# Performance work log

Measured on AMD Instinct MI355X. Metric: run time of the kernel, lower is better.

Reference implementation:

```python
import jax, jax.numpy as jnp
import numpy as np

# Model dims derived from layers=[1024,2048,2048,2048,2048]
B = 4096
SUM_EVEN = 4096  # 0 + 2048 + 2048
SUM_ODD = 4096   # 2048 + 2048
D1 = 2048        # layers[1]: width of Ux
BLK = 2048


def rho(x):
    return jax.nn.sigmoid(4.0 * (x - 0.5))


def make_mask():
    # Staircase block pattern from layer_slices():
    # (rows 0:2048, cols 0:2048), (rows 0:2048, cols 2048:4096), (rows 2048:4096, cols 2048:4096)
    m = np.zeros((SUM_EVEN, SUM_ODD), dtype=np.float32)
    m[0:BLK, 0:BLK] = 1.0
    m[0:BLK, BLK:2 * BLK] = 1.0
    m[BLK:2 * BLK, BLK:2 * BLK] = 1.0
    return jnp.asarray(m)


def setup_inputs() -> dict:
    key = jax.random.key(0)
    k1, k2, k3 = jax.random.split(key, 3)
    xavier_std = 0.02  # ~ sqrt(2/(2048+2048)) per block
    W_mask = make_mask()
    W_tensor = jax.random.normal(k1, (SUM_EVEN, SUM_ODD), jnp.float32) * xavier_std
    W_tensor = W_tensor * W_mask  # enforce staircase sparsity at init
    return {
        "Ux": jax.random.normal(k2, (B, D1), jnp.float32),
        "s": jax.random.normal(k3, (B, SUM_EVEN), jnp.float32),
        "W_tensor": W_tensor,
        "b_even": jnp.zeros((1, SUM_EVEN), jnp.float32),
        "b_odd": jnp.zeros((1, SUM_ODD), jnp.float32),
        "W_mask": W_mask,
    }


def reference(Ux, s, W_tensor, b_even, b_odd, W_mask):
    # s_new = rho(rho(s) @ W + b_odd [+ Ux on first D1 cols]) @ W.T + b_even
    W = W_tensor * W_mask  # masked staircase matrix
    s_odd = rho(s) @ W + b_odd                 # [B, SUM_ODD]
    s_odd = s_odd.at[:, :D1].add(Ux)           # x only feeds first hidden layer
    return rho(s_odd) @ W.T + b_even           # [B, SUM_EVEN]
```

## Files before the change

### kernel.cpp

```cpp
#include <hip/hip_runtime.h>
#include <hip/hip_bf16.h>


#define N_DIM 4096
#define D1_DIM 2048

typedef short short8 __attribute__((ext_vector_type(8)));
typedef float f32x4 __attribute__((ext_vector_type(4)));

__device__ __forceinline__ float rho_f(float x) {
    return 1.0f / (1.0f + __expf(2.0f - 4.0f * x));
}

__device__ __forceinline__ unsigned short f2bf(float x) {
    unsigned int u = __builtin_bit_cast(unsigned int, x);
    u += 0x7fffu + ((u >> 16) & 1u);
    return (unsigned short)(u >> 16);
}

__device__ __forceinline__ void gl_lds16(const unsigned short* g, void* l) {
    __builtin_amdgcn_global_load_lds(
        (const __attribute__((address_space(1))) void*)g,
        (__attribute__((address_space(3))) void*)l, 16, 0, 0);
}

__global__ void prep_rs_kernel(const float* __restrict__ s,
                               unsigned short* __restrict__ Rs, int n8) {
    int t = blockIdx.x * blockDim.x + threadIdx.x;
    int stride = gridDim.x * blockDim.x;
    for (int i = t; i < n8; i += stride) {
        float4 a = ((const float4*)s)[2 * i];
        float4 b = ((const float4*)s)[2 * i + 1];
        unsigned int r0 = f2bf(rho_f(a.x)) | ((unsigned int)f2bf(rho_f(a.y)) << 16);
        unsigned int r1 = f2bf(rho_f(a.z)) | ((unsigned int)f2bf(rho_f(a.w)) << 16);
        unsigned int r2 = f2bf(rho_f(b.x)) | ((unsigned int)f2bf(rho_f(b.y)) << 16);
        unsigned int r3 = f2bf(rho_f(b.z)) | ((unsigned int)f2bf(rho_f(b.w)) << 16);
        uint4 o; o.x = r0; o.y = r1; o.z = r2; o.w = r3;
        ((uint4*)Rs)[i] = o;
    }
}

__global__ void prep_w_kernel(const float* __restrict__ W,
                              unsigned short* __restrict__ Wb,
                              unsigned short* __restrict__ WTb) {
    if (blockIdx.y * 32 >= D1_DIM && blockIdx.x * 32 < D1_DIM) return;
    __shared__ unsigned short t[32][33];
    int x = blockIdx.x * 32 + threadIdx.x;
    #pragma unroll
    for (int r = 0; r < 4; r++) {
        int y = blockIdx.y * 32 + threadIdx.y + r * 8;
        size_t idx = (size_t)y * N_DIM + x;
        unsigned short b = f2bf(W[idx]);
        Wb[idx] = b;
        t[threadIdx.y + r * 8][threadIdx.x] = b;
    }
    __syncthreads();
    #pragma unroll
    for (int r = 0; r < 4; r++) {
        int yy = threadIdx.y + r * 8;
        int orow = blockIdx.x * 32 + yy;
        int ocol = blockIdx.y * 32 + threadIdx.x;
        WTb[(size_t)orow * N_DIM + ocol] = t[threadIdx.x][yy];
    }
}

template<int MODE>
__global__ __launch_bounds__(512, 2) void gemm_kernel(
    const unsigned short* __restrict__ A,
    const unsigned short* __restrict__ Bt,
    void* __restrict__ Out,
    const float* __restrict__ Ux,
    const float* __restrict__ bias) {
    __shared__ __align__(16) char lds[163840];

    const int id = blockIdx.x;
    const int wg = ((id & 7) << 5) | (id >> 3);
    const int by = wg >> 4, bx = wg & 15;
    const int brow = by << 8, bcol = bx << 8;

    const int tid = threadIdx.x;
    const int w = tid >> 6;
    const int L = tid & 63;
    const int wr = w >> 2;
    const int wc = w & 3;
    const int fr = L & 15;
    const int fq = L >> 4;
    const int swz = fr & 7;

    int kbeg, kend;
    if (MODE == 1) { kbeg = 0; kend = (bcol < D1_DIM) ? D1_DIM : N_DIM; }
    else           { kbeg = (bcol < D1_DIM) ? 0 : D1_DIM; kend = N_DIM; }

    const int srl = w * 8 + (L >> 3);
    const int schunk8 = ((L & 7) ^ (L >> 3)) << 3;
    const int wbase = w * 1024;
#define STAGE2(mat, gb, h, kcol, base) do {                                    \
        const unsigned short* g0_ = (mat) +                                    \
            (size_t)((gb) + (h) * 128 + srl) * N_DIM + (kcol) + schunk8;       \
        gl_lds16(g0_, lds + (base) + (h) * 16384 + wbase);                     \
        gl_lds16(g0_ + 64 * N_DIM, lds + (base) + (h) * 16384 + 8192 + wbase); \
    } while (0)

    short8 af[2][4], bf0[2][2], bf1[2][2];
#define LDA_Q(ab, qm) do {                                                     \
        _Pragma("unroll") for (int s_ = 0; s_ < 2; ++s_)                       \
        _Pragma("unroll") for (int m_ = 0; m_ < 4; ++m_) {                     \
            const int R_ = wr * 128 + (qm) * 64 + m_ * 16 + fr;                \
            af[s_][m_] = *(const short8*)(lds + (ab) + R_ * 128 +              \
                (((4 * s_ + fq) ^ swz) << 4)); }                               \
    } while (0)
#define LDB_Q(bb, qn, dst) do {                                                \
        _Pragma("unroll") for (int s_ = 0; s_ < 2; ++s_)                       \
        _Pragma("unroll") for (int n_ = 0; n_ < 2; ++n_) {                     \
            const int R_ = wc * 64 + (qn) * 32 + n_ * 16 + fr;                 \
            dst[s_][n_] = *(const short8*)(lds + (bb) + R_ * 128 +             \
                (((4 * s_ + fq) ^ swz) << 4)); }                               \
    } while (0)

    f32x4 acc[8][4];
    #pragma unroll
    for (int i = 0; i < 8; i++)
        #pragma unroll
        for (int j = 0; j < 4; j++)
            acc[i][j] = (f32x4){0.f, 0.f, 0.f, 0.f};

#define MFMA_Q(qm, qn, bfr) do {                                               \
        __builtin_amdgcn_s_setprio(1);                                         \
        _Pragma("unroll") for (int s_ = 0; s_ < 2; ++s_)                       \
        _Pragma("unroll") for (int m_ = 0; m_ < 4; ++m_)                       \
        _Pragma("unroll") for (int n_ = 0; n_ < 2; ++n_)                       \
            acc[(qm) * 4 + m_][(qn) * 2 + n_] =                                \
                __builtin_amdgcn_mfma_f32_16x16x32_bf16(                       \
                    af[s_][m_], bfr[s_][n_], acc[(qm) * 4 + m_][(qn) * 2 + n_],\
                    0, 0, 0);                                                  \
        __builtin_amdgcn_s_setprio(0);                                         \
    } while (0)

#define LGKM0() do { asm volatile("s_waitcnt lgkmcnt(0)" ::: "memory");        \
                     __builtin_amdgcn_sched_barrier(0); } while (0)
#define BAR() __builtin_amdgcn_s_barrier()

    const int nk = (kend - kbeg) >> 6;
    const int km = nk - 1;

    {
        const int k0 = kbeg;
        const int k1 = kbeg + ((1 & km) << 6);
        STAGE2(A, brow, 0, k0, 0);       STAGE2(A, brow, 1, k0, 0);
        STAGE2(Bt, bcol, 0, k0, 98304);  STAGE2(Bt, bcol, 1, k0, 98304);
        STAGE2(A, brow, 0, k1, 32768);   STAGE2(A, brow, 1, k1, 32768);
        STAGE2(Bt, bcol, 0, k1, 131072); STAGE2(Bt, bcol, 1, k1, 131072);
        asm volatile("s_waitcnt vmcnt(8)" ::: "memory");
        BAR();
    }

    int ai = 0, si = 2, bi = 0;
    for (int t = 0; t < nk; ++t) {
        const int aB = ai * 32768;
        const int sA = si * 32768;
        const int bB = 98304 + bi * 32768;
        const int ka = kbeg + (((t + 2) & km) << 6);

        LDA_Q(aB, 0); LDB_Q(bB, 0, bf0);
        STAGE2(A, brow, 0, ka, sA);
        BAR(); LGKM0();
        MFMA_Q(0, 0, bf0);
        BAR();

        LDB_Q(bB, 1, bf1);
        STAGE2(A, brow, 1, ka, sA);
        BAR(); LGKM0();
        MFMA_Q(0, 1, bf1);
        BAR();

        LDA_Q(aB, 1);
        STAGE2(Bt, bcol, 0, ka, bB);
        BAR(); LGKM0();
        MFMA_Q(1, 1, bf1);
        BAR();

        STAGE2(Bt, bcol, 1, ka, bB);
        asm volatile("s_waitcnt vmcnt(8)" ::: "memory");
        BAR();
        __builtin_amdgcn_sched_barrier(0);
        MFMA_Q(1, 0, bf0);
        BAR();

        ai++; if (ai == 3) ai = 0;
        si++; if (si == 3) si = 0;
        bi ^= 1;
    }
    asm volatile("s_waitcnt vmcnt(0)" ::: "memory");

    const bool hasUx = (MODE == 1) && (bcol < D1_DIM);
    #pragma unroll
    for (int qm = 0; qm < 2; qm++)
        #pragma unroll
        for (int m = 0; m < 4; m++) {
            const int row0 = brow + wr * 128 + qm * 64 + m * 16 + fq * 4;
            #pragma unroll
            for (int qn = 0; qn < 2; qn++)
                #pragma unroll
                for (int n = 0; n < 2; n++) {
                    const int col = bcol + wc * 64 + qn * 32 + n * 16 + fr;
                    const float bv = bias[col];
                    #pragma unroll
                    for (int r = 0; r < 4; r++) {
                        const int row = row0 + r;
                        float v = acc[qm * 4 + m][qn * 2 + n][r] + bv;
                        if (MODE == 1) {
                            if (hasUx) v += Ux[(size_t)row * D1_DIM + col];
                            ((unsigned short*)Out)[(size_t)row * N_DIM + col] =
                                f2bf(rho_f(v));
                        } else {
                            ((float*)Out)[(size_t)row * N_DIM + col] = v;
                        }
                    }
                }
        }
#undef STAGE2
#undef LDA_Q
#undef LDB_Q
#undef MFMA_Q
#undef LGKM0
#undef BAR
}

extern "C" void kernel_launch(void* const* d_in, const int* in_sizes, int n_in,
                              void* d_out, int out_size, void* d_ws, size_t ws_size,
                              hipStream_t stream) {
    const float* Ux     = (const float*)d_in[0];
    const float* s      = (const float*)d_in[1];
    const float* W      = (const float*)d_in[2];
    const float* b_even = (const float*)d_in[3];
    const float* b_odd  = (const float*)d_in[4];

    char* ws = (char*)d_ws;
    const size_t SZ = (size_t)N_DIM * N_DIM * 2;
    unsigned short* Rs  = (unsigned short*)(ws);
    unsigned short* R2  = (unsigned short*)(ws + SZ);
    unsigned short* Wb  = (unsigned short*)(ws + 2 * SZ);
    unsigned short* WTb = (unsigned short*)(ws + 3 * SZ);

    prep_rs_kernel<<<2048, 256, 0, stream>>>(s, Rs, (N_DIM * N_DIM) / 8);
    prep_w_kernel<<<dim3(128, 128), dim3(32, 8), 0, stream>>>(W, Wb, WTb);
    gemm_kernel<1><<<256, 512, 0, stream>>>(Rs, WTb, (void*)R2, Ux, b_odd);
    gemm_kernel<2><<<256, 512, 0, stream>>>(R2, Wb, d_out, Ux, b_even);
}
```

Baseline: 273.9 us.

## Issue all LDS fragment loads up front and cut per-iteration barriers

```diff
diff --git a/kernel.cpp b/kernel.cpp
--- a/kernel.cpp
+++ b/kernel.cpp
@@ -101,12 +101,12 @@
         gl_lds16(g0_ + 64 * N_DIM, lds + (base) + (h) * 16384 + 8192 + wbase); \
     } while (0)
 
-    short8 af[2][4], bf0[2][2], bf1[2][2];
-#define LDA_Q(ab, qm) do {                                                     \
+    short8 af0[2][4], af1[2][4], bf0[2][2], bf1[2][2];
+#define LDA_Q(ab, qm, dst) do {                                                \
         _Pragma("unroll") for (int s_ = 0; s_ < 2; ++s_)                       \
         _Pragma("unroll") for (int m_ = 0; m_ < 4; ++m_) {                     \
             const int R_ = wr * 128 + (qm) * 64 + m_ * 16 + fr;                \
-            af[s_][m_] = *(const short8*)(lds + (ab) + R_ * 128 +              \
+            dst[s_][m_] = *(const short8*)(lds + (ab) + R_ * 128 +             \
                 (((4 * s_ + fq) ^ swz) << 4)); }                               \
     } while (0)
 #define LDB_Q(bb, qn, dst) do {                                                \
@@ -124,20 +124,21 @@
         for (int j = 0; j < 4; j++)
             acc[i][j] = (f32x4){0.f, 0.f, 0.f, 0.f};
 
-#define MFMA_Q(qm, qn, bfr) do {                                               \
+#define MFMA_Q(afr, bfr, qm, qn) do {                                          \
         __builtin_amdgcn_s_setprio(1);                                         \
         _Pragma("unroll") for (int s_ = 0; s_ < 2; ++s_)                       \
         _Pragma("unroll") for (int m_ = 0; m_ < 4; ++m_)                       \
         _Pragma("unroll") for (int n_ = 0; n_ < 2; ++n_)                       \
             acc[(qm) * 4 + m_][(qn) * 2 + n_] =                                \
                 __builtin_amdgcn_mfma_f32_16x16x32_bf16(                       \
-                    af[s_][m_], bfr[s_][n_], acc[(qm) * 4 + m_][(qn) * 2 + n_],\
+                    afr[s_][m_], bfr[s_][n_], acc[(qm) * 4 + m_][(qn) * 2 + n_],\
                     0, 0, 0);                                                  \
         __builtin_amdgcn_s_setprio(0);                                         \
     } while (0)
 
-#define LGKM0() do { asm volatile("s_waitcnt lgkmcnt(0)" ::: "memory");        \
-                     __builtin_amdgcn_sched_barrier(0); } while (0)
+#define SBAR0() __builtin_amdgcn_sched_barrier(0)
+#define LGKM(n) do { asm volatile("s_waitcnt lgkmcnt(" #n ")" ::: "memory");   \
+                     SBAR0(); } while (0)
 #define BAR() __builtin_amdgcn_s_barrier()
 
     const int nk = (kend - kbeg) >> 6;
@@ -154,41 +155,34 @@
         BAR();
     }
 
-    int ai = 0, si = 2, bi = 0;
+    int ai = 0, si = 2;
     for (int t = 0; t < nk; ++t) {
         const int aB = ai * 32768;
         const int sA = si * 32768;
-        const int bB = 98304 + bi * 32768;
+        const int bB = 98304 + (t & 1) * 32768;
         const int ka = kbeg + (((t + 2) & km) << 6);
 
-        LDA_Q(aB, 0); LDB_Q(bB, 0, bf0);
+        LDA_Q(aB, 0, af0); SBAR0();
+        LDB_Q(bB, 0, bf0); SBAR0();
+        LDB_Q(bB, 1, bf1); SBAR0();
+        LDA_Q(aB, 1, af1); SBAR0();
         STAGE2(A, brow, 0, ka, sA);
-        BAR(); LGKM0();
-        MFMA_Q(0, 0, bf0);
+        STAGE2(A, brow, 1, ka, sA);
+
+        LGKM(12);
+        MFMA_Q(af0, bf0, 0, 0);
+        LGKM(8);
+        MFMA_Q(af0, bf1, 0, 1);
         BAR();
-
-        LDB_Q(bB, 1, bf1);
-        STAGE2(A, brow, 1, ka, sA);
-        BAR(); LGKM0();
-        MFMA_Q(0, 1, bf1);
-        BAR();
-
-        LDA_Q(aB, 1);
         STAGE2(Bt, bcol, 0, ka, bB);
-        BAR(); LGKM0();
-        MFMA_Q(1, 1, bf1);
-        BAR();
-
         STAGE2(Bt, bcol, 1, ka, bB);
+        LGKM(0);
+        MFMA_Q(af1, bf0, 1, 0);
+        MFMA_Q(af1, bf1, 1, 1);
         asm volatile("s_waitcnt vmcnt(8)" ::: "memory");
         BAR();
-        __builtin_amdgcn_sched_barrier(0);
-        MFMA_Q(1, 0, bf0);
-        BAR();
-
         ai++; if (ai == 3) ai = 0;
         si++; if (si == 3) si = 0;
-        bi ^= 1;
     }
     asm volatile("s_waitcnt vmcnt(0)" ::: "memory");
 
@@ -222,7 +216,8 @@
 #undef LDA_Q
 #undef LDB_Q
 #undef MFMA_Q
-#undef LGKM0
+#undef SBAR0
+#undef LGKM
 #undef BAR
 }
 
```

Result: faster. 266.3 us (-2.7%).
